# Kernel optimization log

Measured on AMD Instinct MI355X. Metric: run time of the kernel, lower is better.

The kernel has to match this reference:

```python
import jax, jax.numpy as jnp
import numpy as np

B, T, C = 16, 512, 768
MULT = 4
D_IN = C * MULT          # 3072
HIDDEN = 1024
N_DATES = 16
STACK_SIZE, STACK_STRIDE = 4, 2
MAX_F = 512
N_MASK_TYPES = 5
N_SESSIONS = 4
SCALE = HIDDEN ** 0.5


def setup_inputs() -> dict:
    key = jax.random.key(0)
    ks = jax.random.split(key, 12)
    inp = {
        "spikes": jax.random.normal(ks[0], (B, T, C), dtype=jnp.float32),
        "spikes_mask": jnp.ones((B, T), dtype=jnp.int64),
        "spikes_timestamp": jax.random.randint(ks[1], (B, T), 0, 255).astype(jnp.int64),
        "date_idx": jax.random.randint(ks[2], (B,), 0, N_DATES).astype(jnp.int64),
        "mask_idx": 1,
        "session_idx": 3,
        # params
        "W_embed": jax.random.normal(ks[3], (N_DATES, D_IN, C), dtype=jnp.float32) * 0.02,
        "b_embed": jax.random.normal(ks[4], (N_DATES, D_IN), dtype=jnp.float32) * 0.02,
        "W_stack": jax.random.normal(ks[5], (HIDDEN, D_IN * STACK_SIZE), dtype=jnp.float32) * 0.02,
        "b_stack": jax.random.normal(ks[6], (HIDDEN,), dtype=jnp.float32) * 0.02,
        "pos_table": jax.random.normal(ks[7], (MAX_F, HIDDEN), dtype=jnp.float32) * 0.02,
        "prompt_table": jax.random.normal(ks[8], (N_MASK_TYPES, HIDDEN), dtype=jnp.float32) * 0.02,
        "session_table": jax.random.normal(ks[9], (N_SESSIONS, HIDDEN), dtype=jnp.float32) * 0.02,
    }
    return inp


def reference(spikes, spikes_mask, spikes_timestamp, date_idx, mask_idx, session_idx,
              W_embed, b_embed, W_stack, b_stack, pos_table, prompt_table, session_table):
    Bb = spikes.shape[0]
    # adapt branch: per-sample expert Linear, done as one gather + batched GEMM
    W = W_embed[date_idx]                      # [B, D_IN, C]
    b = b_embed[date_idx]                      # [B, D_IN]
    x = jnp.einsum('btc,bdc->btd', spikes, W) + b[:, None, :]   # [B, T, D_IN]
    x = jax.nn.gelu(x, approximate=False) * SCALE
    # unfold-based stacking: sliding windows over time
    L = (T - STACK_SIZE) // STACK_STRIDE + 1   # 255
    starts = jnp.arange(L) * STACK_STRIDE
    widx = starts[:, None] + jnp.arange(STACK_SIZE)             # [L, size]
    win = x[:, widx, :]                                         # [B, L, size, D_IN]
    stacked = win.reshape(Bb, L, STACK_SIZE * D_IN)
    x = stacked @ W_stack.T + b_stack                           # [B, L, HIDDEN]
    ts = spikes_timestamp[:, :L]
    mask = jnp.prod(spikes_mask[:, widx], axis=-1)              # [B, L]
    # positional embedding
    x = x + pos_table[ts]
    # prompt token
    x = jnp.concatenate(
        [jnp.broadcast_to(prompt_table[mask_idx][None, None, :], (Bb, 1, HIDDEN)), x], axis=1)
    mask = jnp.pad(mask, ((0, 0), (1, 0)), constant_values=1)
    ts = jnp.concatenate([jnp.zeros((Bb, 1), ts.dtype), ts + 1], axis=1)
    # session token
    x = jnp.concatenate(
        [jnp.broadcast_to(session_table[session_idx][None, None, :], (Bb, 1, HIDDEN)), x], axis=1)
    mask = jnp.pad(mask, ((0, 0), (1, 0)), constant_values=1)
    ts = jnp.concatenate([jnp.zeros((Bb, 1), ts.dtype), ts + 1], axis=1)
    # dropout is identity in eval
    return x, mask, ts
```

## Files before the change

### kernel.cpp

```cpp
#include <hip/hip_runtime.h>
#include <hip/hip_bf16.h>

#define BATCH   16
#define TT      512
#define CC      768
#define D_IN    3072
#define HIDDEN  1024
#define LL      255
#define OUTROWS 257
#define KSTACK  12288
#define N_DATES 16

typedef float f32x4 __attribute__((ext_vector_type(4)));
typedef __bf16 bf16x8 __attribute__((ext_vector_type(8)));
typedef unsigned short u16;

__device__ __forceinline__ u16 f2bf(float f) {
    unsigned u = __builtin_bit_cast(unsigned, f);
    u = (u + 0x7FFFu + ((u >> 16) & 1u)) >> 16;
    return (u16)u;
}

__device__ __forceinline__ bf16x8 lds_read8(const u16* p) {
    return __builtin_bit_cast(bf16x8, *(const uint4*)p);
}

__device__ __forceinline__ void gload16(const u16* g, u16* l) {
    __builtin_amdgcn_global_load_lds(
        (const __attribute__((address_space(1))) void*)g,
        (__attribute__((address_space(3))) void*)l, 16, 0, 0);
}

__global__ __launch_bounds__(256) void cvt_wstack(const float* __restrict__ W, u16* __restrict__ out) {
    size_t i = ((size_t)blockIdx.x * 256 + threadIdx.x) * 4;
    size_t stride = (size_t)gridDim.x * 256 * 4;
    for (; i < (size_t)HIDDEN * KSTACK; i += stride) {
        float4 v = *(const float4*)(W + i);
        ushort4 o = make_ushort4(f2bf(v.x), f2bf(v.y), f2bf(v.z), f2bf(v.w));
        *(ushort4*)(out + i) = o;
    }
}

__global__ __launch_bounds__(256) void cvt_spikes(const float* __restrict__ in, u16* __restrict__ out) {
    size_t i = ((size_t)blockIdx.x * 256 + threadIdx.x) * 4;
    size_t stride = (size_t)gridDim.x * 256 * 4;
    for (; i < (size_t)BATCH * TT * CC; i += stride) {
        float4 v = *(const float4*)(in + i);
        ushort4 o = make_ushort4(f2bf(v.x), f2bf(v.y), f2bf(v.z), f2bf(v.w));
        *(ushort4*)(out + i) = o;
    }
}

__global__ __launch_bounds__(64) void date_flags(const int* __restrict__ date_idx, int* __restrict__ flags) {
    const int tid = threadIdx.x;
    if (tid < N_DATES) flags[tid] = 0;
    __syncthreads();
    if (tid < BATCH) flags[date_idx[tid]] = 1;
}

__global__ __launch_bounds__(256) void cvt_wembed(const float* __restrict__ W,
                                                  const int* __restrict__ flags,
                                                  u16* __restrict__ out) {
    const int date = blockIdx.y;
    if (!flags[date]) return;
    const size_t bofs = (size_t)date * D_IN * CC;
    const size_t i = bofs + ((size_t)blockIdx.x * 256 + threadIdx.x) * 4;
    float4 v = *(const float4*)(W + i);
    ushort4 o = make_ushort4(f2bf(v.x), f2bf(v.y), f2bf(v.z), f2bf(v.w));
    *(ushort4*)(out + i) = o;
}


__global__ __launch_bounds__(256, 4) void gemm1_bf(const u16* __restrict__ spk,
                                                   const u16* __restrict__ wemb,
                                                   const float* __restrict__ b_embed,
                                                   const int* __restrict__ date_idx,
                                                   u16* __restrict__ x1) {
    const int nwg = 2 * 24 * BATCH;
    const int cpx = nwg / 8;
    const int f   = blockIdx.x;
    const int swz = (f & 7) * cpx + (f >> 3);
    const int bb  = swz / 48;
    const int rem = swz % 48;
    const int m0  = (rem / 24) * 256;
    const int n0  = (rem % 24) * 128;

    const int date = date_idx[bb];
    const u16* A  = spk  + (size_t)bb   * TT * CC;
    const u16* Bw = wemb + (size_t)date * D_IN * CC;
    const int S = CC / 32;

    __shared__ u16 Asm[3][128 * 64];
    __shared__ u16 Bsm[3][64 * 64];

    const int tid  = threadIdx.x;
    const int lane = tid & 63;
    const int wave = tid >> 6;
    const int wm = wave >> 1;
    const int wn = wave & 1;

    const int lrow  = lane >> 3;
    const int scol  = ((lane & 7) ^ lrow) << 3;
    const int chalf = scol >> 5;
    const int gk    = scol & 31;

    f32x4 acc[8][4] = {};

    auto STAGE = [&](int slice, int slot) {
        const int k0 = slice * 32;
        u16* Ad = Asm[slot];
        u16* Bd = Bsm[slot];
        #pragma unroll
        for (int p = 0; p < 4; ++p) {
            const int rbase = (wave + 4 * p) * 8;
            const int tr = 2 * (rbase + lrow) + chalf;
            gload16(A + (size_t)(m0 + tr) * CC + k0 + gk, Ad + rbase * 64);
        }
        #pragma unroll
        for (int p = 0; p < 2; ++p) {
            const int rbase = (wave + 4 * p) * 8;
            const int tr = 2 * (rbase + lrow) + chalf;
            gload16(Bw + (size_t)(n0 + tr) * CC + k0 + gk, Bd + rbase * 64);
        }
    };

    const int krow  = lane & 15;
    const int kcol  = (lane >> 4) << 3;
    const int cfrag = (kcol + ((krow & 1) << 5)) ^ ((krow >> 1) << 3);
    const int urow  = krow >> 1;

    STAGE(0, 0); STAGE(1, 1);
    int cur = 0;
    for (int t = 0; t < S; ++t) {
        if (t + 1 < S) { asm volatile("s_waitcnt vmcnt(6)" ::: "memory"); }
        else           { asm volatile("s_waitcnt vmcnt(0)" ::: "memory"); }
        __builtin_amdgcn_s_barrier();
        const u16* Ab = Asm[cur];
        const u16* Bb = Bsm[cur];
        bf16x8 af[8], bfr[4];
        #pragma unroll
        for (int i = 0; i < 8; ++i)
            af[i] = lds_read8(&Ab[(wm * 64 + i * 8 + urow) * 64 + cfrag]);
        #pragma unroll
        for (int j = 0; j < 4; ++j)
            bfr[j] = lds_read8(&Bb[(wn * 32 + j * 8 + urow) * 64 + cfrag]);
        if (t + 2 < S) {
            const int slot2 = (cur + 2 >= 3) ? cur - 1 : cur + 2;
            STAGE(t + 2, slot2);
        }
        __builtin_amdgcn_s_setprio(1);
        #pragma unroll
        for (int i = 0; i < 8; ++i)
            #pragma unroll
            for (int j = 0; j < 4; ++j)
                acc[i][j] = __builtin_amdgcn_mfma_f32_16x16x32_bf16(af[i], bfr[j], acc[i][j], 0, 0, 0);
        __builtin_amdgcn_s_setprio(0);
        cur = (cur + 1 >= 3) ? 0 : cur + 1;
    }

    const float* be = b_embed + (size_t)date * D_IN;
    #pragma unroll
    for (int i = 0; i < 8; ++i) {
        #pragma unroll
        for (int j = 0; j < 4; ++j) {
            const int col  = n0 + wn * 64 + j * 16 + (lane & 15);
            const float bias = be[col];
            const int rbase = m0 + wm * 128 + i * 16 + ((lane >> 4) << 2);
            #pragma unroll
            for (int q = 0; q < 4; ++q) {
                float v = acc[i][j][q] + bias;
                float g = 0.5f * v * (1.0f + erff(v * 0.70710678118654752f)) * 32.0f;
                x1[(size_t)bb * TT * D_IN + (size_t)(rbase + q) * D_IN + col] = f2bf(g);
            }
        }
    }
}

__global__ __launch_bounds__(256) void gemm1_f32(const float* __restrict__ spikes,
                                                 const float* __restrict__ W_embed,
                                                 const float* __restrict__ b_embed,
                                                 const int* __restrict__ date_idx,
                                                 u16* __restrict__ x1) {
    const int m0 = blockIdx.x * 128;
    const int n0 = blockIdx.y * 128;
    const int bb = blockIdx.z;
    const int date = date_idx[bb];
    const float* A  = spikes  + (size_t)bb  * TT * CC;
    const float* Bw = W_embed + (size_t)date * D_IN * CC;

    __shared__ u16 As[128 * 64];
    __shared__ u16 Bs[128 * 64];

    const int tid  = threadIdx.x;
    const int lane = tid & 63;
    const int wave = tid >> 6;
    const int wm = wave >> 1, wn = wave & 1;

    f32x4 acc[4][4] = {};

    for (int k0 = 0; k0 < CC; k0 += 64) {
        {
            const int c4 = tid & 15;
            int r = tid >> 4;
            #pragma unroll
            for (int p = 0; p < 8; ++p, r += 16) {
                float4 va = *(const float4*)(A  + (size_t)(m0 + r) * CC + k0 + c4 * 4);
                float4 vb = *(const float4*)(Bw + (size_t)(n0 + r) * CC + k0 + c4 * 4);
                const int col = c4 * 4;
                const int idx = r * 64 + (col ^ ((r & 7) << 3));
                *(ushort4*)(&As[idx]) = make_ushort4(f2bf(va.x), f2bf(va.y), f2bf(va.z), f2bf(va.w));
                *(ushort4*)(&Bs[idx]) = make_ushort4(f2bf(vb.x), f2bf(vb.y), f2bf(vb.z), f2bf(vb.w));
            }
        }
        __syncthreads();
        #pragma unroll
        for (int kk = 0; kk < 64; kk += 32) {
            bf16x8 af[4], bfr[4];
            const int krow = lane & 15;
            const int kcol = kk + ((lane >> 4) << 3);
            #pragma unroll
            for (int i = 0; i < 4; ++i) {
                const int ra = wm * 64 + i * 16 + krow;
                af[i]  = lds_read8(&As[ra * 64 + (kcol ^ ((ra & 7) << 3))]);
                const int rb = wn * 64 + i * 16 + krow;
                bfr[i] = lds_read8(&Bs[rb * 64 + (kcol ^ ((rb & 7) << 3))]);
            }
            #pragma unroll
            for (int i = 0; i < 4; ++i)
                #pragma unroll
                for (int j = 0; j < 4; ++j)
                    acc[i][j] = __builtin_amdgcn_mfma_f32_16x16x32_bf16(af[i], bfr[j], acc[i][j], 0, 0, 0);
        }
        __syncthreads();
    }

    const float* be = b_embed + (size_t)date * D_IN;
    #pragma unroll
    for (int i = 0; i < 4; ++i) {
        #pragma unroll
        for (int j = 0; j < 4; ++j) {
            const int col  = n0 + wn * 64 + j * 16 + (lane & 15);
            const float bias = be[col];
            const int rbase = m0 + wm * 64 + i * 16 + ((lane >> 4) << 2);
            #pragma unroll
            for (int q = 0; q < 4; ++q) {
                float v = acc[i][j][q] + bias;
                float g = 0.5f * v * (1.0f + erff(v * 0.70710678118654752f)) * 32.0f;
                x1[(size_t)bb * TT * D_IN + (size_t)(rbase + q) * D_IN + col] = f2bf(g);
            }
        }
    }
}

template <bool WRITE_PART>
__global__ __launch_bounds__(256, 4) void gemm2(const u16* __restrict__ x1,
                                                const u16* __restrict__ Wbf,
                                                float* __restrict__ part,
                                                const float* __restrict__ b_stack,
                                                const float* __restrict__ pos_table,
                                                const int* __restrict__ tstamp,
                                                float* __restrict__ out,
                                                int KS) {
    const int nwg = 8 * KS * BATCH;
    const int cpx = nwg / 8;
    const int f   = blockIdx.x;
    const int swz = (f & 7) * cpx + (f >> 3);
    const int bb  = swz / (8 * KS);
    const int rem = swz % (8 * KS);
    const int ks  = rem / 8;
    const int n0  = (rem % 8) * 128;

    const int KCH  = KSTACK / KS;
    const int kbeg = ks * KCH;
    const int S    = KCH / 32;
    const u16* Xb = x1 + (size_t)bb * TT * D_IN;

    __shared__ u16 Asm[3][128 * 64];
    __shared__ u16 Bsm[3][64 * 64];

    const int tid  = threadIdx.x;
    const int lane = tid & 63;
    const int wave = tid >> 6;
    const int wm = wave >> 1;
    const int wn = wave & 1;

    const int lrow  = lane >> 3;
    const int scol  = ((lane & 7) ^ lrow) << 3;
    const int chalf = scol >> 5;
    const int gk    = scol & 31;

    f32x4 acc[8][4] = {};

    auto STAGE = [&](int slice, int slot) {
        const int k0 = kbeg + slice * 32;
        const int s  = k0 / D_IN;
        const int d0 = k0 % D_IN;
        u16* Ad = Asm[slot];
        u16* Bd = Bsm[slot];
        #pragma unroll
        for (int p = 0; p < 4; ++p) {
            const int rbase = (wave + 4 * p) * 8;
            const int tr = 2 * (rbase + lrow) + chalf;
            gload16(Xb + (size_t)(2 * tr + s) * D_IN + d0 + gk, Ad + rbase * 64);
        }
        #pragma unroll
        for (int p = 0; p < 2; ++p) {
            const int rbase = (wave + 4 * p) * 8;
            const int tr = 2 * (rbase + lrow) + chalf;
            gload16(Wbf + (size_t)(n0 + tr) * KSTACK + k0 + gk, Bd + rbase * 64);
        }
    };

    const int krow  = lane & 15;
    const int kcol  = (lane >> 4) << 3;
    const int cfrag = (kcol + ((krow & 1) << 5)) ^ ((krow >> 1) << 3);
    const int urow  = krow >> 1;

    STAGE(0, 0); STAGE(1, 1);
    int cur = 0;
    for (int t = 0; t < S; ++t) {
        if (t + 1 < S) { asm volatile("s_waitcnt vmcnt(6)" ::: "memory"); }
        else           { asm volatile("s_waitcnt vmcnt(0)" ::: "memory"); }
        __builtin_amdgcn_s_barrier();
        const u16* Ab = Asm[cur];
        const u16* Bb = Bsm[cur];
        bf16x8 af[8], bfr[4];
        #pragma unroll
        for (int i = 0; i < 8; ++i)
            af[i] = lds_read8(&Ab[(wm * 64 + i * 8 + urow) * 64 + cfrag]);
        #pragma unroll
        for (int j = 0; j < 4; ++j)
            bfr[j] = lds_read8(&Bb[(wn * 32 + j * 8 + urow) * 64 + cfrag]);
        if (t + 2 < S) {
            const int slot2 = (cur + 2 >= 3) ? cur - 1 : cur + 2;
            STAGE(t + 2, slot2);
        }
        __builtin_amdgcn_s_setprio(1);
        #pragma unroll
        for (int i = 0; i < 8; ++i)
            #pragma unroll
            for (int j = 0; j < 4; ++j)
                acc[i][j] = __builtin_amdgcn_mfma_f32_16x16x32_bf16(af[i], bfr[j], acc[i][j], 0, 0, 0);
        __builtin_amdgcn_s_setprio(0);
        cur = (cur + 1 >= 3) ? 0 : cur + 1;
    }

    if (WRITE_PART) {
        float* pt = part + ((size_t)(ks * BATCH + bb) * 256) * HIDDEN;
        #pragma unroll
        for (int i = 0; i < 8; ++i) {
            #pragma unroll
            for (int j = 0; j < 4; ++j) {
                const int col = n0 + wn * 64 + j * 16 + (lane & 15);
                const int rb  = wm * 128 + i * 16 + ((lane >> 4) << 2);
                #pragma unroll
                for (int q = 0; q < 4; ++q)
                    pt[(size_t)(rb + q) * HIDDEN + col] = acc[i][j][q];
            }
        }
    } else {
        #pragma unroll
        for (int i = 0; i < 8; ++i) {
            #pragma unroll
            for (int j = 0; j < 4; ++j) {
                const int col = n0 + wn * 64 + j * 16 + (lane & 15);
                const int lb  = wm * 128 + i * 16 + ((lane >> 4) << 2);
                #pragma unroll
                for (int q = 0; q < 4; ++q) {
                    const int l = lb + q;
                    if (l < LL) {
                        const int tsv = tstamp[bb * TT + l];
                        float v = acc[i][j][q] + b_stack[col] + pos_table[(size_t)tsv * HIDDEN + col];
                        out[(size_t)bb * OUTROWS * HIDDEN + (size_t)(2 + l) * HIDDEN + col] = v;
                    }
                }
            }
        }
    }
}

__global__ __launch_bounds__(256) void reduce_ep(const float* __restrict__ part,
                                                 const float* __restrict__ b_stack,
                                                 const float* __restrict__ pos_table,
                                                 const int* __restrict__ tstamp,
                                                 float* __restrict__ out,
                                                 int KS) {
    const int idx = blockIdx.x * 256 + threadIdx.x;
    const int c4  = idx & (HIDDEN / 4 - 1);
    const int r   = idx >> 8;
    if (r >= BATCH * LL) return;
    const int l  = r % LL;
    const int bb = r / LL;
    float4 v = make_float4(0.f, 0.f, 0.f, 0.f);
    for (int ks = 0; ks < KS; ++ks) {
        float4 p = *(const float4*)(part + ((size_t)(ks * BATCH + bb) * 256 + l) * HIDDEN + c4 * 4);
        v.x += p.x; v.y += p.y; v.z += p.z; v.w += p.w;
    }
    const int tsv = tstamp[bb * TT + l];
    float4 bs = *(const float4*)(b_stack + c4 * 4);
    float4 ps = *(const float4*)(pos_table + (size_t)tsv * HIDDEN + c4 * 4);
    v.x += bs.x + ps.x; v.y += bs.y + ps.y; v.z += bs.z + ps.z; v.w += bs.w + ps.w;
    *(float4*)(out + ((size_t)bb * OUTROWS + 2 + l) * HIDDEN + c4 * 4) = v;
}

__global__ __launch_bounds__(256) void epilogue_misc(const int* __restrict__ smask,
                                                     const int* __restrict__ tstamp,
                                                     const int* __restrict__ mask_idx_p,
                                                     const int* __restrict__ session_idx_p,
                                                     const float* __restrict__ prompt_table,
                                                     const float* __restrict__ session_table,
                                                     float* __restrict__ out) {
    const int bb = blockIdx.x;
    const int tid = threadIdx.x;
    const int mi = mask_idx_p[0];
    const int si = session_idx_p[0];
    float* xb = out + (size_t)bb * OUTROWS * HIDDEN;
    for (int i = tid; i < HIDDEN; i += 256) {
        xb[i]          = session_table[(size_t)si * HIDDEN + i];
        xb[HIDDEN + i] = prompt_table[(size_t)mi * HIDDEN + i];
    }
    float* maskout = out + (size_t)BATCH * OUTROWS * HIDDEN + (size_t)bb * OUTROWS;
    float* tsout   = out + (size_t)BATCH * OUTROWS * HIDDEN + (size_t)BATCH * OUTROWS + (size_t)bb * OUTROWS;
    for (int j = tid; j < OUTROWS; j += 256) {
        if (j == 0)      { maskout[0] = 1.0f; tsout[0] = 0.0f; }
        else if (j == 1) { maskout[1] = 1.0f; tsout[1] = 1.0f; }
        else {
            const int l = j - 2;
            int m = 1;
            #pragma unroll
            for (int s = 0; s < 4; ++s) m *= smask[bb * TT + 2 * l + s];
            maskout[j] = (float)m;
            tsout[j]   = (float)(tstamp[bb * TT + l] + 2);
        }
    }
}

extern "C" void kernel_launch(void* const* d_in, const int* in_sizes, int n_in,
                              void* d_out, int out_size, void* d_ws, size_t ws_size,
                              hipStream_t stream) {
    const float* spikes      = (const float*)d_in[0];
    const int*   spikes_mask = (const int*)d_in[1];
    const int*   tstamp      = (const int*)d_in[2];
    const int*   date_idx    = (const int*)d_in[3];
    const int*   mask_idx    = (const int*)d_in[4];
    const int*   session_idx = (const int*)d_in[5];
    const float* W_embed     = (const float*)d_in[6];
    const float* b_embed     = (const float*)d_in[7];
    const float* W_stack     = (const float*)d_in[8];
    const float* b_stack     = (const float*)d_in[9];
    const float* pos_table   = (const float*)d_in[10];
    const float* prompt_tab  = (const float*)d_in[11];
    const float* session_tab = (const float*)d_in[12];
    float* out = (float*)d_out;

    const size_t X1_B   = (size_t)BATCH * TT * D_IN * 2;
    const size_t WBF_B  = (size_t)HIDDEN * KSTACK * 2;
    const size_t PART_B = (size_t)BATCH * 256 * HIDDEN * 4;
    const size_t FLAGS_B = 4096;
    const size_t SPK_B  = (size_t)BATCH * TT * CC * 2;
    const size_t WEMB_B = (size_t)N_DATES * D_IN * CC * 2;
    const size_t BASE   = X1_B + WBF_B;
    const size_t UNION_BF = FLAGS_B + SPK_B + WEMB_B;

    u16*   x1    = (u16*)d_ws;
    u16*   Wbf   = (u16*)((char*)d_ws + X1_B);
    int*   flags = (int*)((char*)d_ws + BASE);
    u16*   spkbf = (u16*)((char*)d_ws + BASE + FLAGS_B);
    u16*   wembf = (u16*)((char*)d_ws + BASE + FLAGS_B + SPK_B);
    float* part  = (float*)((char*)d_ws + BASE);

    const bool use_bf = (ws_size >= BASE + UNION_BF);
    int KS = 0;
    if (use_bf) KS = 4;
    else {
        size_t rem = (ws_size > BASE) ? (ws_size - BASE) : 0;
        KS = (int)(rem / PART_B); if (KS > 4) KS = 4;
    }

    cvt_wstack<<<2048, 256, 0, stream>>>(W_stack, Wbf);

    if (use_bf) {
        date_flags<<<1, 64, 0, stream>>>(date_idx, flags);
        cvt_spikes<<<2048, 256, 0, stream>>>(spikes, spkbf);
        cvt_wembed<<<dim3(D_IN * CC / 4 / 256, N_DATES), 256, 0, stream>>>(W_embed, flags, wembf);
        gemm1_bf<<<2 * 24 * BATCH, 256, 0, stream>>>(spkbf, wembf, b_embed, date_idx, x1);
    } else {
        gemm1_f32<<<dim3(TT / 128, D_IN / 128, BATCH), 256, 0, stream>>>(spikes, W_embed, b_embed, date_idx, x1);
    }

    if (KS > 0) {
        gemm2<true><<<8 * KS * BATCH, 256, 0, stream>>>(x1, Wbf, part, b_stack, pos_table, tstamp, out, KS);
        reduce_ep<<<(BATCH * LL * (HIDDEN / 4) + 255) / 256, 256, 0, stream>>>(part, b_stack, pos_table, tstamp, out, KS);
    } else {
        gemm2<false><<<8 * 1 * BATCH, 256, 0, stream>>>(x1, Wbf, part, b_stack, pos_table, tstamp, out, 1);
    }
    epilogue_misc<<<BATCH, 256, 0, stream>>>(spikes_mask, tstamp, mask_idx, session_idx,
                                             prompt_tab, session_tab, out);
}
```

Baseline: 273.5 us.

## Widen gemm1 tile to 256x192 with double-buffered LDS and streamed A fragments

Changes the first GEMM tile from 256x128 to 256x192 columns, so the grid becomes 512 workgroups (one wave of work on the device) and each workgroup reuses its A tile across more output columns. The LDS pipeline drops from triple to double buffering, with a second barrier before refilling the slot just consumed. A fragments are now read inside the MFMA loop rather than all up front. This cuts A-tile global and LDS traffic per output but raises accumulator register pressure (launch bounds lowered to 2 waves/SIMD) and adds a barrier, which reduces latency hiding.

Measured after the change: 248.0 us. -9.3%, faster.

```diff
diff --git a/kernel.cpp b/kernel.cpp
--- a/kernel.cpp
+++ b/kernel.cpp
@@ -70,28 +70,27 @@
     *(ushort4*)(out + i) = o;
 }
 
-
-__global__ __launch_bounds__(256, 4) void gemm1_bf(const u16* __restrict__ spk,
+__global__ __launch_bounds__(256, 2) void gemm1_bf(const u16* __restrict__ spk,
                                                    const u16* __restrict__ wemb,
                                                    const float* __restrict__ b_embed,
                                                    const int* __restrict__ date_idx,
                                                    u16* __restrict__ x1) {
-    const int nwg = 2 * 24 * BATCH;
+    const int nwg = 512;
     const int cpx = nwg / 8;
     const int f   = blockIdx.x;
     const int swz = (f & 7) * cpx + (f >> 3);
-    const int bb  = swz / 48;
-    const int rem = swz % 48;
-    const int m0  = (rem / 24) * 256;
-    const int n0  = (rem % 24) * 128;
+    const int bb  = swz >> 5;
+    const int rem = swz & 31;
+    const int m0  = (rem >> 4) * 256;
+    const int n0  = (rem & 15) * 192;
 
     const int date = date_idx[bb];
     const u16* A  = spk  + (size_t)bb   * TT * CC;
     const u16* Bw = wemb + (size_t)date * D_IN * CC;
     const int S = CC / 32;
 
-    __shared__ u16 Asm[3][128 * 64];
-    __shared__ u16 Bsm[3][64 * 64];
+    __shared__ u16 Asm[2][128 * 64];
+    __shared__ u16 Bsm[2][96 * 64];
 
     const int tid  = threadIdx.x;
     const int lane = tid & 63;
@@ -104,21 +103,21 @@
     const int chalf = scol >> 5;
     const int gk    = scol & 31;
 
-    f32x4 acc[8][4] = {};
+    f32x4 acc[8][6] = {};
 
     auto STAGE = [&](int slice, int slot) {
         const int k0 = slice * 32;
         u16* Ad = Asm[slot];
         u16* Bd = Bsm[slot];
         #pragma unroll
-        for (int p = 0; p < 4; ++p) {
-            const int rbase = (wave + 4 * p) * 8;
+        for (int i = 0; i < 4; ++i) {
+            const int rbase = wave * 32 + i * 8;
             const int tr = 2 * (rbase + lrow) + chalf;
             gload16(A + (size_t)(m0 + tr) * CC + k0 + gk, Ad + rbase * 64);
         }
         #pragma unroll
-        for (int p = 0; p < 2; ++p) {
-            const int rbase = (wave + 4 * p) * 8;
+        for (int i = 0; i < 3; ++i) {
+            const int rbase = wave * 24 + i * 8;
             const int tr = 2 * (rbase + lrow) + chalf;
             gload16(Bw + (size_t)(n0 + tr) * CC + k0 + gk, Bd + rbase * 64);
         }
@@ -130,40 +129,35 @@
     const int urow  = krow >> 1;
 
     STAGE(0, 0); STAGE(1, 1);
-    int cur = 0;
     for (int t = 0; t < S; ++t) {
-        if (t + 1 < S) { asm volatile("s_waitcnt vmcnt(6)" ::: "memory"); }
+        if (t + 1 < S) { asm volatile("s_waitcnt vmcnt(7)" ::: "memory"); }
         else           { asm volatile("s_waitcnt vmcnt(0)" ::: "memory"); }
         __builtin_amdgcn_s_barrier();
-        const u16* Ab = Asm[cur];
-        const u16* Bb = Bsm[cur];
-        bf16x8 af[8], bfr[4];
-        #pragma unroll
-        for (int i = 0; i < 8; ++i)
-            af[i] = lds_read8(&Ab[(wm * 64 + i * 8 + urow) * 64 + cfrag]);
-        #pragma unroll
-        for (int j = 0; j < 4; ++j)
-            bfr[j] = lds_read8(&Bb[(wn * 32 + j * 8 + urow) * 64 + cfrag]);
-        if (t + 2 < S) {
-            const int slot2 = (cur + 2 >= 3) ? cur - 1 : cur + 2;
-            STAGE(t + 2, slot2);
-        }
+        const u16* Ab = Asm[t & 1];
+        const u16* Bb = Bsm[t & 1];
+        bf16x8 bfr[6];
+        #pragma unroll
+        for (int j = 0; j < 6; ++j)
+            bfr[j] = lds_read8(&Bb[(wn * 48 + j * 8 + urow) * 64 + cfrag]);
         __builtin_amdgcn_s_setprio(1);
         #pragma unroll
-        for (int i = 0; i < 8; ++i)
-            #pragma unroll
-            for (int j = 0; j < 4; ++j)
-                acc[i][j] = __builtin_amdgcn_mfma_f32_16x16x32_bf16(af[i], bfr[j], acc[i][j], 0, 0, 0);
+        for (int i = 0; i < 8; ++i) {
+            bf16x8 af = lds_read8(&Ab[(wm * 64 + i * 8 + urow) * 64 + cfrag]);
+            #pragma unroll
+            for (int j = 0; j < 6; ++j)
+                acc[i][j] = __builtin_amdgcn_mfma_f32_16x16x32_bf16(af, bfr[j], acc[i][j], 0, 0, 0);
+        }
         __builtin_amdgcn_s_setprio(0);
-        cur = (cur + 1 >= 3) ? 0 : cur + 1;
+        __builtin_amdgcn_s_barrier();
+        if (t + 2 < S) STAGE(t + 2, t & 1);
     }
 
     const float* be = b_embed + (size_t)date * D_IN;
     #pragma unroll
     for (int i = 0; i < 8; ++i) {
         #pragma unroll
-        for (int j = 0; j < 4; ++j) {
-            const int col  = n0 + wn * 64 + j * 16 + (lane & 15);
+        for (int j = 0; j < 6; ++j) {
+            const int col  = n0 + wn * 96 + j * 16 + (lane & 15);
             const float bias = be[col];
             const int rbase = m0 + wm * 128 + i * 16 + ((lane >> 4) << 2);
             #pragma unroll
@@ -483,7 +477,7 @@
         date_flags<<<1, 64, 0, stream>>>(date_idx, flags);
         cvt_spikes<<<2048, 256, 0, stream>>>(spikes, spkbf);
         cvt_wembed<<<dim3(D_IN * CC / 4 / 256, N_DATES), 256, 0, stream>>>(W_embed, flags, wembf);
-        gemm1_bf<<<2 * 24 * BATCH, 256, 0, stream>>>(spkbf, wembf, b_embed, date_idx, x1);
+        gemm1_bf<<<512, 256, 0, stream>>>(spkbf, wembf, b_embed, date_idx, x1);
     } else {
         gemm1_f32<<<dim3(TT / 128, D_IN / 128, BATCH), 256, 0, stream>>>(spikes, W_embed, b_embed, date_idx, x1);
     }
```
